# Performance work log

Hardware: AMD Instinct MI355X
Metric: run time of the kernel (lower is better)

## Reference

```python
import jax, jax.numpy as jnp
import numpy as np

B, C, H, W = 8, 256, 64, 64
GROUPS = 8
EPS = 1e-5


def setup_inputs() -> dict:
    key = jax.random.key(0)
    ks = jax.random.split(key, 10)
    s = 1.0 / np.sqrt(C)
    return {
        "x": jax.random.normal(ks[0], (B, C, H, W), dtype=jnp.float32),
        "gn_gamma": jnp.ones((C,), jnp.float32),
        "gn_beta": jnp.zeros((C,), jnp.float32),
        "wq": jax.random.uniform(ks[1], (C, C), jnp.float32, -s, s),
        "bq": jax.random.uniform(ks[2], (C,), jnp.float32, -s, s),
        "wk": jax.random.uniform(ks[3], (C, C), jnp.float32, -s, s),
        "bk": jax.random.uniform(ks[4], (C,), jnp.float32, -s, s),
        "wv": jax.random.uniform(ks[5], (C, C), jnp.float32, -s, s),
        "bv": jax.random.uniform(ks[6], (C,), jnp.float32, -s, s),
        "wp": jax.random.uniform(ks[7], (C, C), jnp.float32, -s, s),
        "bp": jax.random.uniform(ks[8], (C,), jnp.float32, -s, s),
    }


def _group_norm(x, gamma, beta):
    b, c, h, w = x.shape
    xg = x.reshape(b, GROUPS, c // GROUPS, h, w)
    mu = jnp.mean(xg, axis=(2, 3, 4), keepdims=True)
    var = jnp.mean(jnp.square(xg - mu), axis=(2, 3, 4), keepdims=True)
    xn = ((xg - mu) * jax.lax.rsqrt(var + EPS)).reshape(b, c, h, w)
    return xn * gamma[None, :, None, None] + beta[None, :, None, None]


def reference(x, gn_gamma, gn_beta, wq, bq, wk, bk, wv, bv, wp, bp):
    b, c, h, w = x.shape
    xn = _group_norm(x, gn_gamma, gn_beta)
    xf = xn.reshape(b, c, h * w)  # [b, c, n]
    # 1x1 Conv1d == per-position channel matmul
    q = jnp.einsum('oc,bcn->bon', wq, xf) + bq[None, :, None]
    k = jnp.einsum('oc,bcn->bon', wk, xf) + bk[None, :, None]
    v = jnp.einsum('oc,bcn->bon', wv, xf) + bv[None, :, None]
    scale = 1.0 / jnp.sqrt(jnp.asarray(c, xf.dtype))
    # attn[b,i,j] = softmax_j(q[:,i]^T k[:,j] / sqrt(c))
    attn = jax.nn.softmax(jnp.einsum('bci,bcj->bij', q, k) * scale, axis=-1)
    # out[b,c,i] = sum_j v[b,c,j] * attn[b,i,j]
    out = jnp.einsum('bcj,bij->bci', v, attn)
    out = jnp.einsum('oc,bcn->bon', wp, out) + bp[None, :, None]
    return x + out.reshape(b, c, h, w)
```

## Files before the change

### kernel.cpp

```cpp
#include <hip/hip_runtime.h>


typedef __bf16 bf16x8 __attribute__((ext_vector_type(8)));
typedef __bf16 bf16x4 __attribute__((ext_vector_type(4)));
typedef float floatx4 __attribute__((ext_vector_type(4)));
typedef float floatx16 __attribute__((ext_vector_type(16)));

constexpr int Bb = 8, Cc_ = 256, HW = 4096;
constexpr int BNT = Bb * HW;

__device__ __forceinline__ void load_lds16(const void* g, void* l) {
  __builtin_amdgcn_global_load_lds((const __attribute__((address_space(1))) void*)g,
                                   (__attribute__((address_space(3))) void*)l, 16, 0, 0);
}

#define MEMFENCE asm volatile("" ::: "memory")
__device__ __forceinline__ void bar_sync() {
  MEMFENCE;
  __builtin_amdgcn_s_barrier();
  MEMFENCE;
}

__global__ __launch_bounds__(256) void gn_part(const float* __restrict__ x,
                                               float* __restrict__ part) {
  int sub = blockIdx.x & 7;
  int bg = blockIdx.x >> 3;
  const float4* p = (const float4*)(x + (size_t)bg * 131072 + (size_t)sub * 16384);
  int tid = threadIdx.x;
  float s = 0.f, ss = 0.f;
#pragma unroll
  for (int i = 0; i < 16; ++i) {
    float4 v = p[i * 256 + tid];
    s += v.x + v.y + v.z + v.w;
    ss += v.x * v.x + v.y * v.y + v.z * v.z + v.w * v.w;
  }
  for (int off = 32; off; off >>= 1) { s += __shfl_down(s, off); ss += __shfl_down(ss, off); }
  __shared__ float red[8];
  int wv = tid >> 6, ln = tid & 63;
  if (ln == 0) { red[wv] = s; red[4 + wv] = ss; }
  __syncthreads();
  if (tid == 0) {
    part[blockIdx.x * 2] = red[0] + red[1] + red[2] + red[3];
    part[blockIdx.x * 2 + 1] = red[4] + red[5] + red[6] + red[7];
  }
}

__global__ __launch_bounds__(256) void gn_norm_t(const float* __restrict__ x,
                                                 const float* __restrict__ part,
                                                 const float* __restrict__ gamma,
                                                 const float* __restrict__ beta,
                                                 __bf16* __restrict__ Xt) {
  __shared__ float tile[64][65];
  __shared__ float sst[4];
  int b = blockIdx.z, c0 = blockIdx.y * 64, n0 = blockIdx.x * 64;
  int tid = threadIdx.x;
  if (tid < 2) {
    int g = b * 8 + (c0 >> 5) + tid;
    float s = 0.f, ss = 0.f;
#pragma unroll
    for (int k = 0; k < 8; ++k) { s += part[(g * 8 + k) * 2]; ss += part[(g * 8 + k) * 2 + 1]; }
    float mean = s / 131072.f;
    float var = ss / 131072.f - mean * mean;
    sst[tid * 2] = mean;
    sst[tid * 2 + 1] = rsqrtf(var + 1e-5f);
  }
  int cl = tid >> 4, nl = (tid & 15) * 4;
  const float* xb = x + ((size_t)b * Cc_ + c0) * HW + n0;
#pragma unroll
  for (int i = 0; i < 4; ++i) {
    int c = cl + i * 16;
    float4 v = *(const float4*)&xb[(size_t)c * HW + nl];
    tile[c][nl] = v.x; tile[c][nl + 1] = v.y; tile[c][nl + 2] = v.z; tile[c][nl + 3] = v.w;
  }
  __syncthreads();
#pragma unroll
  for (int i = 0; i < 16; ++i) {
    int idx = i * 256 + tid;
    int n = idx >> 6, c = idx & 63;
    int gc = c0 + c;
    float mean = sst[(c >> 5) * 2], rstd = sst[(c >> 5) * 2 + 1];
    float v = (tile[c][n] - mean) * rstd * gamma[gc] + beta[gc];
    Xt[((size_t)b * HW + n0 + n) * Cc_ + gc] = (__bf16)v;
  }
}

__global__ __launch_bounds__(256) void pack_w(const float* __restrict__ wq, const float* __restrict__ wk,
                                              const float* __restrict__ wv, const float* __restrict__ wp,
                                              const float* __restrict__ bq, const float* __restrict__ bk,
                                              const float* __restrict__ bv, const float* __restrict__ bp,
                                              __bf16* __restrict__ Wqk, __bf16* __restrict__ Wv,
                                              __bf16* __restrict__ Wp, float* __restrict__ Bqk,
                                              float* __restrict__ Bv, float* __restrict__ Bp) {
  int i = blockIdx.x * 256 + threadIdx.x;
  if (i < 65536) {
    Wqk[i] = (__bf16)wq[i];
    Wqk[65536 + i] = (__bf16)wk[i];
    Wv[i] = (__bf16)wv[i];
    Wp[i] = (__bf16)wp[i];
  }
  if (i < 256) { Bqk[i] = bq[i]; Bqk[256 + i] = bk[i]; Bv[i] = bv[i]; Bp[i] = bp[i]; }
}

template <int BM, int BN, int WM, int WN, int EPI>
__global__ __launch_bounds__(256) void gemm_bt(
    const __bf16* __restrict__ A, int lda,
    const __bf16* __restrict__ B, int ldb,
    __bf16* __restrict__ C, int ldc,
    int K, float scale,
    const float* __restrict__ bias,
    const float* __restrict__ resid,
    float* __restrict__ outF) {
  constexpr int TM = WM / 16, TN = WN / 16;
  __shared__ __bf16 As[BM * 32];
  __shared__ __bf16 Bs[BN * 32];

  const int tid = threadIdx.x;
  const int wave = tid >> 6, lane = tid & 63;
  const int wr = wave >> 1, wc = wave & 1;
  const int quad = lane >> 4, l16 = lane & 15;
  const int m0 = blockIdx.y * BM, n0 = blockIdx.x * BN;
  const int srow = lane >> 2;
  const int scol = (lane & 3) * 8;

  floatx4 acc[TM][TN] = {};

  const int kTiles = K / 32;
  for (int kt = 0; kt < kTiles; ++kt) {
    const int k0 = kt * 32;
    __syncthreads();
#pragma unroll
    for (int i = 0; i < BM / 64; ++i) {
      int row = i * 64 + wave * 16 + srow;
      load_lds16(A + (size_t)(m0 + row) * lda + k0 + scol, &As[(i * 64 + wave * 16) * 32]);
    }
#pragma unroll
    for (int i = 0; i < BN / 64; ++i) {
      int row = i * 64 + wave * 16 + srow;
      load_lds16(B + (size_t)(n0 + row) * ldb + k0 + scol, &Bs[(i * 64 + wave * 16) * 32]);
    }
    __syncthreads();

    bf16x8 af[TM], bfr[TN];
#pragma unroll
    for (int i = 0; i < TM; ++i)
      af[i] = *(const bf16x8*)&As[(wr * WM + i * 16 + l16) * 32 + quad * 8];
#pragma unroll
    for (int j = 0; j < TN; ++j)
      bfr[j] = *(const bf16x8*)&Bs[(wc * WN + j * 16 + l16) * 32 + quad * 8];
#pragma unroll
    for (int i = 0; i < TM; ++i)
#pragma unroll
      for (int j = 0; j < TN; ++j)
        acc[i][j] = __builtin_amdgcn_mfma_f32_16x16x32_bf16(af[i], bfr[j], acc[i][j], 0, 0, 0);
  }

#pragma unroll
  for (int i = 0; i < TM; ++i) {
#pragma unroll
    for (int j = 0; j < TN; ++j) {
      int gc = n0 + wc * WN + j * 16 + l16;
#pragma unroll
      for (int r = 0; r < 4; ++r) {
        int gr = m0 + wr * WM + i * 16 + quad * 4 + r;
        float v = acc[i][j][r] * scale;
        if constexpr (EPI == 1) v += bias[gc];
        if constexpr (EPI == 2) v += bias[gr];
        if constexpr (EPI == 3) {
          int bb = gc >> 12, nn = gc & 4095;
          size_t oidx = (size_t)bb * (Cc_ * HW) + (size_t)gr * HW + nn;
          outF[oidx] = v + bias[gr] + resid[oidx];
        } else {
          C[(size_t)gr * ldc + gc] = (__bf16)v;
        }
      }
    }
  }
}

__global__ __launch_bounds__(512, 2) void flash_attn(const __bf16* __restrict__ QK,
                                                     const __bf16* __restrict__ V,
                                                     __bf16* __restrict__ O) {
  __shared__ __align__(16) __bf16 smem[65536];
  __bf16* Ks = smem;
  __bf16* Vt = smem + 32768;
  __bf16* Pb = smem + 49152;

  const int tid = threadIdx.x;
  const int w = tid >> 6, lane = tid & 63;
  const int l31 = lane & 31, hh = lane >> 5;
  const int b = blockIdx.x & 7;
  const int m0 = (blockIdx.x >> 3) * 128;

  if (w < 4) {
    const int h = w & 1, qp = w >> 1;
    const int ks_slot = lane & 31, ks_rin = lane >> 5;

    bf16x8 qf[2][16];
#pragma unroll
    for (int qt = 0; qt < 2; ++qt) {
      const size_t qrow = (size_t)(b * HW + m0 + qp * 64 + qt * 32 + l31);
#pragma unroll
      for (int kc = 0; kc < 16; ++kc) {
        qf[qt][kc] = *(const bf16x8*)&QK[qrow * 512 + kc * 16 + hh * 8];
#pragma unroll
        for (int e = 0; e < 8; ++e) qf[qt][kc][e] = (__bf16)((float)qf[qt][kc][e] * 0.0625f);
      }
    }
#pragma unroll
    for (int i = 0; i < 8; ++i) {
      int rl = w * 16 + i * 2 + ks_rin;
      load_lds16(QK + (size_t)(b * HW + rl) * 512 + 256 + ((ks_slot ^ (rl & 31)) << 3),
                 &Ks[(w * 16 + i * 2) * 256]);
    }
    asm volatile("s_waitcnt vmcnt(0)" ::: "memory");
    bar_sync();

    float lr0 = 0.f, lr1 = 0.f;
    const int jl = h * 32 + l31;

    for (int t = 0; t < 64; ++t) {
      if (t < 63) {
        __bf16* Kn = Ks + (((t + 1) & 1) << 14);
#pragma unroll
        for (int i = 0; i < 8; ++i) {
          int rl = w * 16 + i * 2 + ks_rin;
          load_lds16(QK + (size_t)(b * HW + (t + 1) * 64 + rl) * 512 + 256 +
                         ((ks_slot ^ (rl & 31)) << 3),
                     &Kn[(w * 16 + i * 2) * 256]);
        }
      }
      const __bf16* krow = &Ks[((t & 1) << 14) + jl * 256];
      floatx16 s0 = {}, s1 = {};
      __builtin_amdgcn_s_setprio(1);
#pragma unroll
      for (int kc = 0; kc < 16; ++kc) {
        bf16x8 kfv = *(const bf16x8*)&krow[((kc * 2 + hh) ^ l31) << 3];
        s0 = __builtin_amdgcn_mfma_f32_32x32x16_bf16(kfv, qf[0][kc], s0, 0, 0, 0);
        s1 = __builtin_amdgcn_mfma_f32_32x32x16_bf16(kfv, qf[1][kc], s1, 0, 0, 0);
      }
      __builtin_amdgcn_s_setprio(0);
      float ls0 = 0.f, ls1 = 0.f;
#pragma unroll
      for (int i = 0; i < 16; ++i) {
        float p0 = __expf(s0[i]); s0[i] = p0; ls0 += p0;
        float p1 = __expf(s1[i]); s1[i] = p1; ls1 += p1;
      }
      lr0 += ls0; lr1 += ls1;
      __bf16* Pt = Pb + ((t & 1) << 13);
#pragma unroll
      for (int g = 0; g < 4; ++g) {
        bf16x4 pk0, pk1;
#pragma unroll
        for (int k = 0; k < 4; ++k) { pk0[k] = (__bf16)s0[g * 4 + k]; pk1[k] = (__bf16)s1[g * 4 + k]; }
        *(bf16x4*)&Pt[(qp * 64 + l31) * 64 + ((((4 * h + g) ^ (l31 & 7)) << 3) + 4 * hh)] = pk0;
        *(bf16x4*)&Pt[(qp * 64 + 32 + l31) * 64 + ((((4 * h + g) ^ (l31 & 7)) << 3) + 4 * hh)] = pk1;
      }
      asm volatile("s_waitcnt vmcnt(0) lgkmcnt(0)" ::: "memory");
      bar_sync();
    }

    float* Lb = (float*)Pb;
    float l20 = lr0 + __shfl_xor(lr0, 32);
    float l21 = lr1 + __shfl_xor(lr1, 32);
    if (hh == 0) {
      Lb[h * 128 + qp * 64 + l31] = l20;
      Lb[h * 128 + qp * 64 + 32 + l31] = l21;
    }
    asm volatile("s_waitcnt lgkmcnt(0)" ::: "memory");
    bar_sync();
    if (w == 0) {
      float* Linv = (float*)Pb + 256;
      Linv[lane] = 1.f / (Lb[lane] + Lb[128 + lane]);
      Linv[64 + lane] = 1.f / (Lb[64 + lane] + Lb[192 + lane]);
    }
    asm volatile("s_waitcnt lgkmcnt(0)" ::: "memory");
    bar_sync();
    bar_sync();
  } else {
    const int ch = w - 4;
    const int vt_slot = lane & 7, vt_rin = lane >> 3;

#pragma unroll
    for (int i = 0; i < 8; ++i) {
      int cl = ch * 64 + i * 8 + vt_rin;
      load_lds16(V + (size_t)cl * BNT + (b * HW + ((vt_slot ^ (cl & 7)) << 3)),
                 &Vt[(ch * 64 + i * 8) * 64]);
    }
    bar_sync();

    floatx16 oacc[4][2] = {};

    for (int t = 0; t < 64; ++t) {
      asm volatile("s_waitcnt vmcnt(0)" ::: "memory");
      if (t > 0) {
        const __bf16* Pp = Pb + (((t - 1) & 1) << 13);
        __builtin_amdgcn_s_setprio(1);
#pragma unroll
        for (int ks = 0; ks < 4; ++ks) {
          bf16x8 pf[4], vf[2];
#pragma unroll
          for (int qt = 0; qt < 4; ++qt)
            pf[qt] = *(const bf16x8*)&Pp[(qt * 32 + l31) * 64 + (((ks * 2 + hh) ^ (l31 & 7)) << 3)];
#pragma unroll
          for (int nt = 0; nt < 2; ++nt) {
            int cl = ch * 64 + nt * 32 + l31;
            vf[nt] = *(const bf16x8*)&Vt[cl * 64 + (((ks * 2 + hh) ^ (cl & 7)) << 3)];
          }
#pragma unroll
          for (int qt = 0; qt < 4; ++qt)
#pragma unroll
            for (int nt = 0; nt < 2; ++nt)
              oacc[qt][nt] = __builtin_amdgcn_mfma_f32_32x32x16_bf16(pf[qt], vf[nt], oacc[qt][nt], 0, 0, 0);
        }
        __builtin_amdgcn_s_setprio(0);
        asm volatile("s_waitcnt lgkmcnt(0)" ::: "memory");
#pragma unroll
        for (int i = 0; i < 8; ++i) {
          int cl = ch * 64 + i * 8 + vt_rin;
          load_lds16(V + (size_t)cl * BNT + (b * HW + t * 64 + ((vt_slot ^ (cl & 7)) << 3)),
                     &Vt[(ch * 64 + i * 8) * 64]);
        }
      }
      bar_sync();
    }

    asm volatile("s_waitcnt vmcnt(0)" ::: "memory");
    {
      const __bf16* Pp = Pb + 8192;
      __builtin_amdgcn_s_setprio(1);
#pragma unroll
      for (int ks = 0; ks < 4; ++ks) {
        bf16x8 pf[4], vf[2];
#pragma unroll
        for (int qt = 0; qt < 4; ++qt)
          pf[qt] = *(const bf16x8*)&Pp[(qt * 32 + l31) * 64 + (((ks * 2 + hh) ^ (l31 & 7)) << 3)];
#pragma unroll
        for (int nt = 0; nt < 2; ++nt) {
          int cl = ch * 64 + nt * 32 + l31;
          vf[nt] = *(const bf16x8*)&Vt[cl * 64 + (((ks * 2 + hh) ^ (cl & 7)) << 3)];
        }
#pragma unroll
        for (int qt = 0; qt < 4; ++qt)
#pragma unroll
          for (int nt = 0; nt < 2; ++nt)
            oacc[qt][nt] = __builtin_amdgcn_mfma_f32_32x32x16_bf16(pf[qt], vf[nt], oacc[qt][nt], 0, 0, 0);
      }
      __builtin_amdgcn_s_setprio(0);
    }
    asm volatile("s_waitcnt lgkmcnt(0)" ::: "memory");
    bar_sync();
    bar_sync();

    const float* Linv = (const float*)Pb + 256;
    __bf16* Os = smem;
#pragma unroll
    for (int qt = 0; qt < 4; ++qt) {
#pragma unroll
      for (int g = 0; g < 4; ++g) {
        floatx4 lv = *(const floatx4*)&Linv[qt * 32 + g * 8 + 4 * hh];
#pragma unroll
        for (int k = 0; k < 4; ++k) {
          int qloc = qt * 32 + g * 8 + 4 * hh + k;
#pragma unroll
          for (int nt = 0; nt < 2; ++nt) {
            int c = ch * 64 + nt * 32 + l31;
            Os[qloc * 256 + c] = (__bf16)(oacc[qt][nt][g * 4 + k] * lv[k]);
          }
        }
      }
    }
    asm volatile("s_waitcnt lgkmcnt(0)" ::: "memory");
    bar_sync();
  }

  const float4* src = (const float4*)smem;
  float4* dst = (float4*)(O + (size_t)(b * HW + m0) * 256);
#pragma unroll
  for (int i = 0; i < 8; ++i) dst[i * 512 + tid] = src[i * 512 + tid];
}

extern "C" void kernel_launch(void* const* d_in, const int* in_sizes, int n_in,
                              void* d_out, int out_size, void* d_ws, size_t ws_size,
                              hipStream_t stream) {
  const float* x = (const float*)d_in[0];
  const float* gamma = (const float*)d_in[1];
  const float* beta = (const float*)d_in[2];
  const float* wq = (const float*)d_in[3];
  const float* bq = (const float*)d_in[4];
  const float* wk = (const float*)d_in[5];
  const float* bk = (const float*)d_in[6];
  const float* wv = (const float*)d_in[7];
  const float* bv = (const float*)d_in[8];
  const float* wp = (const float*)d_in[9];
  const float* bp = (const float*)d_in[10];
  float* out = (float*)d_out;

  char* ws = (char*)d_ws;
  size_t off = 0;
  auto alloc = [&](size_t n) { size_t o = off; off = (off + n + 255) & ~(size_t)255; return o; };
  __bf16* XT = (__bf16*)(ws + alloc((size_t)BNT * Cc_ * 2));
  __bf16* QK = (__bf16*)(ws + alloc((size_t)BNT * 512 * 2));
  __bf16* V  = (__bf16*)(ws + alloc((size_t)Cc_ * BNT * 2));
  __bf16* O  = (__bf16*)(ws + alloc((size_t)BNT * Cc_ * 2));
  __bf16* WQK = (__bf16*)(ws + alloc(512 * 256 * 2));
  __bf16* WV  = (__bf16*)(ws + alloc(256 * 256 * 2));
  __bf16* WP  = (__bf16*)(ws + alloc(256 * 256 * 2));
  float* BQK = (float*)(ws + alloc(512 * 4));
  float* BV  = (float*)(ws + alloc(256 * 4));
  float* BP  = (float*)(ws + alloc(256 * 4));
  float* PART = (float*)(ws + alloc(512 * 2 * 4));

  pack_w<<<dim3(256), dim3(256), 0, stream>>>(wq, wk, wv, wp, bq, bk, bv, bp,
                                              WQK, WV, WP, BQK, BV, BP);
  gn_part<<<dim3(512), dim3(256), 0, stream>>>(x, PART);
  gn_norm_t<<<dim3(64, 4, 8), dim3(256), 0, stream>>>(x, PART, gamma, beta, XT);

  gemm_bt<128, 128, 64, 64, 1><<<dim3(512 / 128, BNT / 128), dim3(256), 0, stream>>>(
      XT, 256, WQK, 256, QK, 512, 256, 1.0f, BQK, nullptr, nullptr);
  gemm_bt<128, 128, 64, 64, 2><<<dim3(BNT / 128, 256 / 128), dim3(256), 0, stream>>>(
      WV, 256, XT, 256, V, BNT, 256, 1.0f, BV, nullptr, nullptr);

  flash_attn<<<dim3(256), dim3(512), 0, stream>>>(QK, V, O);

  gemm_bt<128, 128, 64, 64, 3><<<dim3(BNT / 128, 256 / 128), dim3(256), 0, stream>>>(
      WP, 256, O, 256, nullptr, 0, 256, 1.0f, BP, x, out);
}
```

Before: 291.4 us.

## Restructure flash attention to 32-key tiles with triple-buffered K and merge weight pack into GN kernel

The flash attention kernel now processes 32-key tiles over 128 iterations instead of 64-key tiles. Each QK wave owns 32 query rows outright, so the cross-wave row-sum reduction goes away. K is triple-buffered so prefetch runs two tiles ahead with partial vmcnt waits, and V is double-buffered. This cuts LDS use, which may allow more overlap or occupancy, but doubles the number of barriers and loop iterations. Separately, the weight-pack kernel is folded into the GroupNorm partial-stats launch to save one kernel launch.

```diff
diff --git a/kernel.cpp b/kernel.cpp
--- a/kernel.cpp
+++ b/kernel.cpp
@@ -21,27 +21,44 @@
   MEMFENCE;
 }
 
-__global__ __launch_bounds__(256) void gn_part(const float* __restrict__ x,
-                                               float* __restrict__ part) {
-  int sub = blockIdx.x & 7;
-  int bg = blockIdx.x >> 3;
-  const float4* p = (const float4*)(x + (size_t)bg * 131072 + (size_t)sub * 16384);
+__global__ __launch_bounds__(256) void gn_part_pack(
+    const float* __restrict__ x, float* __restrict__ part,
+    const float* __restrict__ wq, const float* __restrict__ wk,
+    const float* __restrict__ wv, const float* __restrict__ wp,
+    const float* __restrict__ bq, const float* __restrict__ bk,
+    const float* __restrict__ bv, const float* __restrict__ bp,
+    __bf16* __restrict__ Wqk, __bf16* __restrict__ Wv, __bf16* __restrict__ Wp,
+    float* __restrict__ Bqk, float* __restrict__ Bv, float* __restrict__ Bp) {
+  __shared__ float red[8];
   int tid = threadIdx.x;
-  float s = 0.f, ss = 0.f;
-#pragma unroll
-  for (int i = 0; i < 16; ++i) {
-    float4 v = p[i * 256 + tid];
-    s += v.x + v.y + v.z + v.w;
-    ss += v.x * v.x + v.y * v.y + v.z * v.z + v.w * v.w;
-  }
-  for (int off = 32; off; off >>= 1) { s += __shfl_down(s, off); ss += __shfl_down(ss, off); }
-  __shared__ float red[8];
-  int wv = tid >> 6, ln = tid & 63;
-  if (ln == 0) { red[wv] = s; red[4 + wv] = ss; }
-  __syncthreads();
-  if (tid == 0) {
-    part[blockIdx.x * 2] = red[0] + red[1] + red[2] + red[3];
-    part[blockIdx.x * 2 + 1] = red[4] + red[5] + red[6] + red[7];
+  if (blockIdx.x < 512) {
+    int sub = blockIdx.x & 7;
+    int bg = blockIdx.x >> 3;
+    const float4* p = (const float4*)(x + (size_t)bg * 131072 + (size_t)sub * 16384);
+    float s = 0.f, ss = 0.f;
+#pragma unroll
+    for (int i = 0; i < 16; ++i) {
+      float4 v = p[i * 256 + tid];
+      s += v.x + v.y + v.z + v.w;
+      ss += v.x * v.x + v.y * v.y + v.z * v.z + v.w * v.w;
+    }
+    for (int off = 32; off; off >>= 1) { s += __shfl_down(s, off); ss += __shfl_down(ss, off); }
+    int wv_ = tid >> 6, ln = tid & 63;
+    if (ln == 0) { red[wv_] = s; red[4 + wv_] = ss; }
+    __syncthreads();
+    if (tid == 0) {
+      part[blockIdx.x * 2] = red[0] + red[1] + red[2] + red[3];
+      part[blockIdx.x * 2 + 1] = red[4] + red[5] + red[6] + red[7];
+    }
+  } else {
+    int i = (blockIdx.x - 512) * 256 + tid;
+    if (i < 65536) {
+      Wqk[i] = (__bf16)wq[i];
+      Wqk[65536 + i] = (__bf16)wk[i];
+      Wv[i] = (__bf16)wv[i];
+      Wp[i] = (__bf16)wp[i];
+    }
+    if (i < 256) { Bqk[i] = bq[i]; Bqk[256 + i] = bk[i]; Bv[i] = bv[i]; Bp[i] = bp[i]; }
   }
 }
 
@@ -84,23 +101,6 @@
   }
 }
 
-__global__ __launch_bounds__(256) void pack_w(const float* __restrict__ wq, const float* __restrict__ wk,
-                                              const float* __restrict__ wv, const float* __restrict__ wp,
-                                              const float* __restrict__ bq, const float* __restrict__ bk,
-                                              const float* __restrict__ bv, const float* __restrict__ bp,
-                                              __bf16* __restrict__ Wqk, __bf16* __restrict__ Wv,
-                                              __bf16* __restrict__ Wp, float* __restrict__ Bqk,
-                                              float* __restrict__ Bv, float* __restrict__ Bp) {
-  int i = blockIdx.x * 256 + threadIdx.x;
-  if (i < 65536) {
-    Wqk[i] = (__bf16)wq[i];
-    Wqk[65536 + i] = (__bf16)wk[i];
-    Wv[i] = (__bf16)wv[i];
-    Wp[i] = (__bf16)wp[i];
-  }
-  if (i < 256) { Bqk[i] = bq[i]; Bqk[256 + i] = bk[i]; Bv[i] = bv[i]; Bp[i] = bp[i]; }
-}
-
 template <int BM, int BN, int WM, int WN, int EPI>
 __global__ __launch_bounds__(256) void gemm_bt(
     const __bf16* __restrict__ A, int lda,
@@ -180,10 +180,11 @@
 __global__ __launch_bounds__(512, 2) void flash_attn(const __bf16* __restrict__ QK,
                                                      const __bf16* __restrict__ V,
                                                      __bf16* __restrict__ O) {
-  __shared__ __align__(16) __bf16 smem[65536];
-  __bf16* Ks = smem;
-  __bf16* Vt = smem + 32768;
-  __bf16* Pb = smem + 49152;
+  __shared__ __align__(16) __bf16 smem[49408];
+  __bf16* KsB = smem;
+  __bf16* VtB = smem + 24576;
+  __bf16* PbB = smem + 40960;
+  float* Linv = (float*)(smem + 49152);
 
   const int tid = threadIdx.x;
   const int w = tid >> 6, lane = tid & 63;
@@ -192,119 +193,108 @@
   const int m0 = (blockIdx.x >> 3) * 128;
 
   if (w < 4) {
-    const int h = w & 1, qp = w >> 1;
+    const int qp = w;
     const int ks_slot = lane & 31, ks_rin = lane >> 5;
 
-    bf16x8 qf[2][16];
-#pragma unroll
-    for (int qt = 0; qt < 2; ++qt) {
-      const size_t qrow = (size_t)(b * HW + m0 + qp * 64 + qt * 32 + l31);
+    bf16x8 qf[16];
+    {
+      const size_t qrow = (size_t)(b * HW + m0 + qp * 32 + l31);
 #pragma unroll
       for (int kc = 0; kc < 16; ++kc) {
-        qf[qt][kc] = *(const bf16x8*)&QK[qrow * 512 + kc * 16 + hh * 8];
-#pragma unroll
-        for (int e = 0; e < 8; ++e) qf[qt][kc][e] = (__bf16)((float)qf[qt][kc][e] * 0.0625f);
-      }
-    }
-#pragma unroll
-    for (int i = 0; i < 8; ++i) {
-      int rl = w * 16 + i * 2 + ks_rin;
-      load_lds16(QK + (size_t)(b * HW + rl) * 512 + 256 + ((ks_slot ^ (rl & 31)) << 3),
-                 &Ks[(w * 16 + i * 2) * 256]);
-    }
-    asm volatile("s_waitcnt vmcnt(0)" ::: "memory");
-    bar_sync();
-
-    float lr0 = 0.f, lr1 = 0.f;
-    const int jl = h * 32 + l31;
-
-    for (int t = 0; t < 64; ++t) {
-      if (t < 63) {
-        __bf16* Kn = Ks + (((t + 1) & 1) << 14);
-#pragma unroll
-        for (int i = 0; i < 8; ++i) {
-          int rl = w * 16 + i * 2 + ks_rin;
-          load_lds16(QK + (size_t)(b * HW + (t + 1) * 64 + rl) * 512 + 256 +
-                         ((ks_slot ^ (rl & 31)) << 3),
-                     &Kn[(w * 16 + i * 2) * 256]);
-        }
-      }
-      const __bf16* krow = &Ks[((t & 1) << 14) + jl * 256];
-      floatx16 s0 = {}, s1 = {};
+        qf[kc] = *(const bf16x8*)&QK[qrow * 512 + kc * 16 + hh * 8];
+#pragma unroll
+        for (int e = 0; e < 8; ++e) qf[kc][e] = (__bf16)((float)qf[kc][e] * 0.0625f);
+      }
+    }
+#pragma unroll
+    for (int tt = 0; tt < 2; ++tt)
+#pragma unroll
+      for (int i = 0; i < 4; ++i) {
+        int rl = qp * 8 + i * 2 + ks_rin;
+        load_lds16(QK + (size_t)(b * HW + tt * 32 + rl) * 512 + 256 + ((ks_slot ^ rl) << 3),
+                   &KsB[tt * 8192 + (qp * 8 + i * 2) * 256]);
+      }
+    asm volatile("s_waitcnt vmcnt(4)" ::: "memory");
+    bar_sync();
+
+    __bf16 *k0 = KsB, *k1 = KsB + 8192, *k2 = KsB + 16384;
+    float lr = 0.f;
+    const int q = qp * 32 + l31;
+    const int pkey = (l31 >> 1) & 3;
+
+    for (int t = 0; t < 128; ++t) {
+      if (t < 126) {
+#pragma unroll
+        for (int i = 0; i < 4; ++i) {
+          int rl = qp * 8 + i * 2 + ks_rin;
+          load_lds16(QK + (size_t)(b * HW + (t + 2) * 32 + rl) * 512 + 256 + ((ks_slot ^ rl) << 3),
+                     &k2[(qp * 8 + i * 2) * 256]);
+        }
+      }
+      const __bf16* krow = &k0[l31 * 256];
+      floatx16 s = {};
       __builtin_amdgcn_s_setprio(1);
 #pragma unroll
       for (int kc = 0; kc < 16; ++kc) {
         bf16x8 kfv = *(const bf16x8*)&krow[((kc * 2 + hh) ^ l31) << 3];
-        s0 = __builtin_amdgcn_mfma_f32_32x32x16_bf16(kfv, qf[0][kc], s0, 0, 0, 0);
-        s1 = __builtin_amdgcn_mfma_f32_32x32x16_bf16(kfv, qf[1][kc], s1, 0, 0, 0);
+        s = __builtin_amdgcn_mfma_f32_32x32x16_bf16(kfv, qf[kc], s, 0, 0, 0);
       }
       __builtin_amdgcn_s_setprio(0);
-      float ls0 = 0.f, ls1 = 0.f;
-#pragma unroll
-      for (int i = 0; i < 16; ++i) {
-        float p0 = __expf(s0[i]); s0[i] = p0; ls0 += p0;
-        float p1 = __expf(s1[i]); s1[i] = p1; ls1 += p1;
-      }
-      lr0 += ls0; lr1 += ls1;
-      __bf16* Pt = Pb + ((t & 1) << 13);
+      float ls = 0.f;
+#pragma unroll
+      for (int i = 0; i < 16; ++i) { float p = __expf(s[i]); s[i] = p; ls += p; }
+      lr += ls;
+      __bf16* Pt = PbB + ((t & 1) << 12);
 #pragma unroll
       for (int g = 0; g < 4; ++g) {
-        bf16x4 pk0, pk1;
-#pragma unroll
-        for (int k = 0; k < 4; ++k) { pk0[k] = (__bf16)s0[g * 4 + k]; pk1[k] = (__bf16)s1[g * 4 + k]; }
-        *(bf16x4*)&Pt[(qp * 64 + l31) * 64 + ((((4 * h + g) ^ (l31 & 7)) << 3) + 4 * hh)] = pk0;
-        *(bf16x4*)&Pt[(qp * 64 + 32 + l31) * 64 + ((((4 * h + g) ^ (l31 & 7)) << 3) + 4 * hh)] = pk1;
-      }
-      asm volatile("s_waitcnt vmcnt(0) lgkmcnt(0)" ::: "memory");
+        bf16x4 pk;
+#pragma unroll
+        for (int k = 0; k < 4; ++k) pk[k] = (__bf16)s[g * 4 + k];
+        *(bf16x4*)&Pt[q * 32 + ((g ^ pkey) << 3) + 4 * hh] = pk;
+      }
+      if (t < 126) asm volatile("s_waitcnt vmcnt(4) lgkmcnt(0)" ::: "memory");
+      else         asm volatile("s_waitcnt vmcnt(0) lgkmcnt(0)" ::: "memory");
       bar_sync();
-    }
-
-    float* Lb = (float*)Pb;
-    float l20 = lr0 + __shfl_xor(lr0, 32);
-    float l21 = lr1 + __shfl_xor(lr1, 32);
-    if (hh == 0) {
-      Lb[h * 128 + qp * 64 + l31] = l20;
-      Lb[h * 128 + qp * 64 + 32 + l31] = l21;
-    }
-    asm volatile("s_waitcnt lgkmcnt(0)" ::: "memory");
-    bar_sync();
-    if (w == 0) {
-      float* Linv = (float*)Pb + 256;
-      Linv[lane] = 1.f / (Lb[lane] + Lb[128 + lane]);
-      Linv[64 + lane] = 1.f / (Lb[64 + lane] + Lb[192 + lane]);
-    }
+      __bf16* tmp = k0; k0 = k1; k1 = k2; k2 = tmp;
+    }
+
+    float l2 = lr + __shfl_xor(lr, 32);
+    if (hh == 0) Linv[q] = 1.f / l2;
     asm volatile("s_waitcnt lgkmcnt(0)" ::: "memory");
     bar_sync();
     bar_sync();
   } else {
     const int ch = w - 4;
-    const int vt_slot = lane & 7, vt_rin = lane >> 3;
-
-#pragma unroll
-    for (int i = 0; i < 8; ++i) {
-      int cl = ch * 64 + i * 8 + vt_rin;
-      load_lds16(V + (size_t)cl * BNT + (b * HW + ((vt_slot ^ (cl & 7)) << 3)),
-                 &Vt[(ch * 64 + i * 8) * 64]);
+    const int vt_slot = lane & 3, vt_rin = lane >> 2;
+
+#pragma unroll
+    for (int i = 0; i < 4; ++i) {
+      int cl = ch * 64 + i * 16 + vt_rin;
+      load_lds16(V + (size_t)cl * BNT + (b * HW + ((vt_slot ^ ((cl >> 1) & 3)) << 3)),
+                 &VtB[(ch * 64 + i * 16) * 32]);
     }
     bar_sync();
 
     floatx16 oacc[4][2] = {};
 
-    for (int t = 0; t < 64; ++t) {
-      asm volatile("s_waitcnt vmcnt(0)" ::: "memory");
+    for (int t = 0; t < 128; ++t) {
       if (t > 0) {
-        const __bf16* Pp = Pb + (((t - 1) & 1) << 13);
+        asm volatile("s_waitcnt vmcnt(4)" ::: "memory");
+        const __bf16* Pp = PbB + (((t - 1) & 1) << 12);
+        const __bf16* Vc = VtB + (((t - 1) & 1) << 13);
         __builtin_amdgcn_s_setprio(1);
 #pragma unroll
-        for (int ks = 0; ks < 4; ++ks) {
+        for (int ks = 0; ks < 2; ++ks) {
           bf16x8 pf[4], vf[2];
 #pragma unroll
-          for (int qt = 0; qt < 4; ++qt)
-            pf[qt] = *(const bf16x8*)&Pp[(qt * 32 + l31) * 64 + (((ks * 2 + hh) ^ (l31 & 7)) << 3)];
+          for (int qt = 0; qt < 4; ++qt) {
+            int qq = qt * 32 + l31;
+            pf[qt] = *(const bf16x8*)&Pp[qq * 32 + (((ks * 2 + hh) ^ ((qq >> 1) & 3)) << 3)];
+          }
 #pragma unroll
           for (int nt = 0; nt < 2; ++nt) {
             int cl = ch * 64 + nt * 32 + l31;
-            vf[nt] = *(const bf16x8*)&Vt[cl * 64 + (((ks * 2 + hh) ^ (cl & 7)) << 3)];
+            vf[nt] = *(const bf16x8*)&Vc[cl * 32 + (((ks * 2 + hh) ^ ((cl >> 1) & 3)) << 3)];
           }
 #pragma unroll
           for (int qt = 0; qt < 4; ++qt)
@@ -314,11 +304,13 @@
         }
         __builtin_amdgcn_s_setprio(0);
         asm volatile("s_waitcnt lgkmcnt(0)" ::: "memory");
-#pragma unroll
-        for (int i = 0; i < 8; ++i) {
-          int cl = ch * 64 + i * 8 + vt_rin;
-          load_lds16(V + (size_t)cl * BNT + (b * HW + t * 64 + ((vt_slot ^ (cl & 7)) << 3)),
-                     &Vt[(ch * 64 + i * 8) * 64]);
+      }
+      if (t < 127) {
+#pragma unroll
+        for (int i = 0; i < 4; ++i) {
+          int cl = ch * 64 + i * 16 + vt_rin;
+          load_lds16(V + (size_t)cl * BNT + (b * HW + (t + 1) * 32 + ((vt_slot ^ ((cl >> 1) & 3)) << 3)),
+                     &VtB[(((t + 1) & 1) << 13) + (ch * 64 + i * 16) * 32]);
         }
       }
       bar_sync();
@@ -326,18 +318,21 @@
 
     asm volatile("s_waitcnt vmcnt(0)" ::: "memory");
     {
-      const __bf16* Pp = Pb + 8192;
+      const __bf16* Pp = PbB + 4096;
+      const __bf16* Vc = VtB + 8192;
       __builtin_amdgcn_s_setprio(1);
 #pragma unroll
-      for (int ks = 0; ks < 4; ++ks) {
+      for (int ks = 0; ks < 2; ++ks) {
         bf16x8 pf[4], vf[2];
 #pragma unroll
-        for (int qt = 0; qt < 4; ++qt)
-          pf[qt] = *(const bf16x8*)&Pp[(qt * 32 + l31) * 64 + (((ks * 2 + hh) ^ (l31 & 7)) << 3)];
+        for (int qt = 0; qt < 4; ++qt) {
+          int qq = qt * 32 + l31;
+          pf[qt] = *(const bf16x8*)&Pp[qq * 32 + (((ks * 2 + hh) ^ ((qq >> 1) & 3)) << 3)];
+        }
 #pragma unroll
         for (int nt = 0; nt < 2; ++nt) {
           int cl = ch * 64 + nt * 32 + l31;
-          vf[nt] = *(const bf16x8*)&Vt[cl * 64 + (((ks * 2 + hh) ^ (cl & 7)) << 3)];
+          vf[nt] = *(const bf16x8*)&Vc[cl * 32 + (((ks * 2 + hh) ^ ((cl >> 1) & 3)) << 3)];
         }
 #pragma unroll
         for (int qt = 0; qt < 4; ++qt)
@@ -349,9 +344,7 @@
     }
     asm volatile("s_waitcnt lgkmcnt(0)" ::: "memory");
     bar_sync();
-    bar_sync();
-
-    const float* Linv = (const float*)Pb + 256;
+
     __bf16* Os = smem;
 #pragma unroll
     for (int qt = 0; qt < 4; ++qt) {
@@ -410,9 +403,9 @@
   float* BP  = (float*)(ws + alloc(256 * 4));
   float* PART = (float*)(ws + alloc(512 * 2 * 4));
 
-  pack_w<<<dim3(256), dim3(256), 0, stream>>>(wq, wk, wv, wp, bq, bk, bv, bp,
-                                              WQK, WV, WP, BQK, BV, BP);
-  gn_part<<<dim3(512), dim3(256), 0, stream>>>(x, PART);
+  gn_part_pack<<<dim3(768), dim3(256), 0, stream>>>(x, PART, wq, wk, wv, wp,
+                                                    bq, bk, bv, bp,
+                                                    WQK, WV, WP, BQK, BV, BP);
   gn_norm_t<<<dim3(64, 4, 8), dim3(256), 0, stream>>>(x, PART, gamma, beta, XT);
 
   gemm_bt<128, 128, 64, 64, 1><<<dim3(512 / 128, BNT / 128), dim3(256), 0, stream>>>(
```

Result: slower. 308.7 us (+5.9%).

## Stage K/V tiles through registers and fuse weight packing into GN stats kernel

Applied to the files above, without the earlier changes.

In the flash-attention kernel, the direct global-to-LDS loads for K and V tiles are replaced by register prefetch: the next tile is loaded into registers during compute and written to swizzled LDS after the compute of the current tile. This removes the per-iteration vmcnt(0) waits so global latency can overlap the MFMA work, at the cost of extra VGPRs and explicit LDS store instructions. Separately, the weight/bias bf16 packing kernel is merged into the group-norm partial-sum kernel as extra blocks, saving one kernel launch.

```diff
diff --git a/kernel.cpp b/kernel.cpp
--- a/kernel.cpp
+++ b/kernel.cpp
@@ -21,27 +21,44 @@
   MEMFENCE;
 }
 
-__global__ __launch_bounds__(256) void gn_part(const float* __restrict__ x,
-                                               float* __restrict__ part) {
-  int sub = blockIdx.x & 7;
-  int bg = blockIdx.x >> 3;
-  const float4* p = (const float4*)(x + (size_t)bg * 131072 + (size_t)sub * 16384);
+__global__ __launch_bounds__(256) void gn_part_pack(
+    const float* __restrict__ x, float* __restrict__ part,
+    const float* __restrict__ wq, const float* __restrict__ wk,
+    const float* __restrict__ wv, const float* __restrict__ wp,
+    const float* __restrict__ bq, const float* __restrict__ bk,
+    const float* __restrict__ bv, const float* __restrict__ bp,
+    __bf16* __restrict__ Wqk, __bf16* __restrict__ Wv, __bf16* __restrict__ Wp,
+    float* __restrict__ Bqk, float* __restrict__ Bv, float* __restrict__ Bp) {
+  __shared__ float red[8];
   int tid = threadIdx.x;
-  float s = 0.f, ss = 0.f;
-#pragma unroll
-  for (int i = 0; i < 16; ++i) {
-    float4 v = p[i * 256 + tid];
-    s += v.x + v.y + v.z + v.w;
-    ss += v.x * v.x + v.y * v.y + v.z * v.z + v.w * v.w;
-  }
-  for (int off = 32; off; off >>= 1) { s += __shfl_down(s, off); ss += __shfl_down(ss, off); }
-  __shared__ float red[8];
-  int wv = tid >> 6, ln = tid & 63;
-  if (ln == 0) { red[wv] = s; red[4 + wv] = ss; }
-  __syncthreads();
-  if (tid == 0) {
-    part[blockIdx.x * 2] = red[0] + red[1] + red[2] + red[3];
-    part[blockIdx.x * 2 + 1] = red[4] + red[5] + red[6] + red[7];
+  if (blockIdx.x < 512) {
+    int sub = blockIdx.x & 7;
+    int bg = blockIdx.x >> 3;
+    const float4* p = (const float4*)(x + (size_t)bg * 131072 + (size_t)sub * 16384);
+    float s = 0.f, ss = 0.f;
+#pragma unroll
+    for (int i = 0; i < 16; ++i) {
+      float4 v = p[i * 256 + tid];
+      s += v.x + v.y + v.z + v.w;
+      ss += v.x * v.x + v.y * v.y + v.z * v.z + v.w * v.w;
+    }
+    for (int off = 32; off; off >>= 1) { s += __shfl_down(s, off); ss += __shfl_down(ss, off); }
+    int wv_ = tid >> 6, ln = tid & 63;
+    if (ln == 0) { red[wv_] = s; red[4 + wv_] = ss; }
+    __syncthreads();
+    if (tid == 0) {
+      part[blockIdx.x * 2] = red[0] + red[1] + red[2] + red[3];
+      part[blockIdx.x * 2 + 1] = red[4] + red[5] + red[6] + red[7];
+    }
+  } else {
+    int i = (blockIdx.x - 512) * 256 + tid;
+    if (i < 65536) {
+      Wqk[i] = (__bf16)wq[i];
+      Wqk[65536 + i] = (__bf16)wk[i];
+      Wv[i] = (__bf16)wv[i];
+      Wp[i] = (__bf16)wp[i];
+    }
+    if (i < 256) { Bqk[i] = bq[i]; Bqk[256 + i] = bk[i]; Bv[i] = bv[i]; Bp[i] = bp[i]; }
   }
 }
 
@@ -84,23 +101,6 @@
   }
 }
 
-__global__ __launch_bounds__(256) void pack_w(const float* __restrict__ wq, const float* __restrict__ wk,
-                                              const float* __restrict__ wv, const float* __restrict__ wp,
-                                              const float* __restrict__ bq, const float* __restrict__ bk,
-                                              const float* __restrict__ bv, const float* __restrict__ bp,
-                                              __bf16* __restrict__ Wqk, __bf16* __restrict__ Wv,
-                                              __bf16* __restrict__ Wp, float* __restrict__ Bqk,
-                                              float* __restrict__ Bv, float* __restrict__ Bp) {
-  int i = blockIdx.x * 256 + threadIdx.x;
-  if (i < 65536) {
-    Wqk[i] = (__bf16)wq[i];
-    Wqk[65536 + i] = (__bf16)wk[i];
-    Wv[i] = (__bf16)wv[i];
-    Wp[i] = (__bf16)wp[i];
-  }
-  if (i < 256) { Bqk[i] = bq[i]; Bqk[256 + i] = bk[i]; Bv[i] = bv[i]; Bp[i] = bp[i]; }
-}
-
 template <int BM, int BN, int WM, int WN, int EPI>
 __global__ __launch_bounds__(256) void gemm_bt(
     const __bf16* __restrict__ A, int lda,
@@ -206,29 +206,29 @@
         for (int e = 0; e < 8; ++e) qf[qt][kc][e] = (__bf16)((float)qf[qt][kc][e] * 0.0625f);
       }
     }
+    bf16x8 kreg[8];
 #pragma unroll
     for (int i = 0; i < 8; ++i) {
       int rl = w * 16 + i * 2 + ks_rin;
-      load_lds16(QK + (size_t)(b * HW + rl) * 512 + 256 + ((ks_slot ^ (rl & 31)) << 3),
-                 &Ks[(w * 16 + i * 2) * 256]);
-    }
-    asm volatile("s_waitcnt vmcnt(0)" ::: "memory");
+      kreg[i] = *(const bf16x8*)&QK[(size_t)(b * HW + rl) * 512 + 256 + ks_slot * 8];
+    }
+#pragma unroll
+    for (int i = 0; i < 8; ++i) {
+      int rl = w * 16 + i * 2 + ks_rin;
+      *(bf16x8*)&Ks[rl * 256 + ((ks_slot ^ (rl & 31)) << 3)] = kreg[i];
+    }
+#pragma unroll
+    for (int i = 0; i < 8; ++i) {
+      int rl = w * 16 + i * 2 + ks_rin;
+      kreg[i] = *(const bf16x8*)&QK[(size_t)(b * HW + 64 + rl) * 512 + 256 + ks_slot * 8];
+    }
+    asm volatile("s_waitcnt lgkmcnt(0)" ::: "memory");
     bar_sync();
 
     float lr0 = 0.f, lr1 = 0.f;
     const int jl = h * 32 + l31;
 
     for (int t = 0; t < 64; ++t) {
-      if (t < 63) {
-        __bf16* Kn = Ks + (((t + 1) & 1) << 14);
-#pragma unroll
-        for (int i = 0; i < 8; ++i) {
-          int rl = w * 16 + i * 2 + ks_rin;
-          load_lds16(QK + (size_t)(b * HW + (t + 1) * 64 + rl) * 512 + 256 +
-                         ((ks_slot ^ (rl & 31)) << 3),
-                     &Kn[(w * 16 + i * 2) * 256]);
-        }
-      }
       const __bf16* krow = &Ks[((t & 1) << 14) + jl * 256];
       floatx16 s0 = {}, s1 = {};
       __builtin_amdgcn_s_setprio(1);
@@ -255,7 +255,22 @@
         *(bf16x4*)&Pt[(qp * 64 + l31) * 64 + ((((4 * h + g) ^ (l31 & 7)) << 3) + 4 * hh)] = pk0;
         *(bf16x4*)&Pt[(qp * 64 + 32 + l31) * 64 + ((((4 * h + g) ^ (l31 & 7)) << 3) + 4 * hh)] = pk1;
       }
-      asm volatile("s_waitcnt vmcnt(0) lgkmcnt(0)" ::: "memory");
+      if (t < 63) {
+        __bf16* Kn = Ks + (((t + 1) & 1) << 14);
+#pragma unroll
+        for (int i = 0; i < 8; ++i) {
+          int rl = w * 16 + i * 2 + ks_rin;
+          *(bf16x8*)&Kn[rl * 256 + ((ks_slot ^ (rl & 31)) << 3)] = kreg[i];
+        }
+      }
+      if (t < 62) {
+#pragma unroll
+        for (int i = 0; i < 8; ++i) {
+          int rl = w * 16 + i * 2 + ks_rin;
+          kreg[i] = *(const bf16x8*)&QK[(size_t)(b * HW + (t + 2) * 64 + rl) * 512 + 256 + ks_slot * 8];
+        }
+      }
+      asm volatile("s_waitcnt lgkmcnt(0)" ::: "memory");
       bar_sync();
     }
 
@@ -280,18 +295,17 @@
     const int ch = w - 4;
     const int vt_slot = lane & 7, vt_rin = lane >> 3;
 
+    bf16x8 vreg[8];
 #pragma unroll
     for (int i = 0; i < 8; ++i) {
       int cl = ch * 64 + i * 8 + vt_rin;
-      load_lds16(V + (size_t)cl * BNT + (b * HW + ((vt_slot ^ (cl & 7)) << 3)),
-                 &Vt[(ch * 64 + i * 8) * 64]);
+      vreg[i] = *(const bf16x8*)&V[(size_t)cl * BNT + b * HW + vt_slot * 8];
     }
     bar_sync();
 
     floatx16 oacc[4][2] = {};
 
     for (int t = 0; t < 64; ++t) {
-      asm volatile("s_waitcnt vmcnt(0)" ::: "memory");
       if (t > 0) {
         const __bf16* Pp = Pb + (((t - 1) & 1) << 13);
         __builtin_amdgcn_s_setprio(1);
@@ -314,17 +328,23 @@
         }
         __builtin_amdgcn_s_setprio(0);
         asm volatile("s_waitcnt lgkmcnt(0)" ::: "memory");
+      }
+#pragma unroll
+      for (int i = 0; i < 8; ++i) {
+        int cl = ch * 64 + i * 8 + vt_rin;
+        *(bf16x8*)&Vt[cl * 64 + ((vt_slot ^ (cl & 7)) << 3)] = vreg[i];
+      }
+      if (t < 63) {
 #pragma unroll
         for (int i = 0; i < 8; ++i) {
           int cl = ch * 64 + i * 8 + vt_rin;
-          load_lds16(V + (size_t)cl * BNT + (b * HW + t * 64 + ((vt_slot ^ (cl & 7)) << 3)),
-                     &Vt[(ch * 64 + i * 8) * 64]);
-        }
-      }
+          vreg[i] = *(const bf16x8*)&V[(size_t)cl * BNT + b * HW + (t + 1) * 64 + vt_slot * 8];
+        }
+      }
+      asm volatile("s_waitcnt lgkmcnt(0)" ::: "memory");
       bar_sync();
     }
 
-    asm volatile("s_waitcnt vmcnt(0)" ::: "memory");
     {
       const __bf16* Pp = Pb + 8192;
       __builtin_amdgcn_s_setprio(1);
@@ -410,9 +430,9 @@
   float* BP  = (float*)(ws + alloc(256 * 4));
   float* PART = (float*)(ws + alloc(512 * 2 * 4));
 
-  pack_w<<<dim3(256), dim3(256), 0, stream>>>(wq, wk, wv, wp, bq, bk, bv, bp,
-                                              WQK, WV, WP, BQK, BV, BP);
-  gn_part<<<dim3(512), dim3(256), 0, stream>>>(x, PART);
+  gn_part_pack<<<dim3(768), dim3(256), 0, stream>>>(x, PART, wq, wk, wv, wp,
+                                                    bq, bk, bv, bp,
+                                                    WQK, WV, WP, BQK, BV, BP);
   gn_norm_t<<<dim3(64, 4, 8), dim3(256), 0, stream>>>(x, PART, gamma, beta, XT);
 
   gemm_bt<128, 128, 64, 64, 1><<<dim3(512 / 128, BNT / 128), dim3(256), 0, stream>>>(
```

Measured after the change: 285.2 us. 2.1% less time.
